# Performance work log

Measured on AMD Instinct MI355X. Metric: run time of the kernel, lower is better.

The kernel has to match this reference:

```python
import jax, jax.numpy as jnp
import numpy as np

N = 100000   # nodes
E = 1600000  # edges
IN = 32      # in_channels
H = 64       # hidden_channels
L = 16       # latent_dim
G = 64       # graphs in batch


def setup_inputs() -> dict:
    key = jax.random.key(0)
    ks = jax.random.split(key, 20)
    def w(k, shape, fan):
        return jax.random.normal(k, shape, jnp.float32) * (1.0 / np.sqrt(fan))
    inp = {}
    inp["x"] = jax.random.normal(ks[0], (N, IN), jnp.float32)
    inp["edge_index"] = jax.random.randint(ks[1], (2, E), 0, N)
    inp["batch"] = jnp.sort(jax.random.randint(ks[2], (N,), 0, G))
    # encoder GCN convs: in->h, h->h, h->h
    inp["W_enc0"] = w(ks[3], (IN, H), IN); inp["b_enc0"] = jnp.zeros((H,), jnp.float32)
    inp["W_enc1"] = w(ks[4], (H, H), H);   inp["b_enc1"] = jnp.zeros((H,), jnp.float32)
    inp["W_enc2"] = w(ks[5], (H, H), H);   inp["b_enc2"] = jnp.zeros((H,), jnp.float32)
    # latent projection and decoder projection
    inp["W_proj"] = w(ks[6], (H, L), H);   inp["b_proj"] = jnp.zeros((L,), jnp.float32)
    inp["W_dec_proj"] = w(ks[7], (L, H), L); inp["b_dec_proj"] = jnp.zeros((H,), jnp.float32)
    # decoder GCN convs: h->h, h->in
    inp["W_dec0"] = w(ks[8], (H, H), H);   inp["b_dec0"] = jnp.zeros((H,), jnp.float32)
    inp["W_dec1"] = w(ks[9], (H, IN), H);  inp["b_dec1"] = jnp.zeros((IN,), jnp.float32)
    return inp


def gcn_conv(x, W, b, src, dst, dinv):
    xw = x @ W                                   # [N, out]
    coef = (dinv[src] * dinv[dst])[:, None]      # [E, 1]
    out = jax.ops.segment_sum(xw[src] * coef, dst, num_segments=N)
    out = out + xw * (dinv * dinv)[:, None]      # self-loop contribution
    return out + b


def reference(x, edge_index, batch,
              W_enc0, b_enc0, W_enc1, b_enc1, W_enc2, b_enc2,
              W_proj, b_proj, W_dec_proj, b_dec_proj,
              W_dec0, b_dec0, W_dec1, b_dec1):
    src, dst = edge_index[0], edge_index[1]
    # degree with self-loops (computed on target nodes, PyG default)
    deg = jax.ops.segment_sum(jnp.ones((E,), jnp.float32), dst, num_segments=N) + 1.0
    dinv = jax.lax.rsqrt(deg)
    # encoder (eval mode: dropout is identity)
    h = jax.nn.relu(gcn_conv(x, W_enc0, b_enc0, src, dst, dinv))
    h = jax.nn.relu(gcn_conv(h, W_enc1, b_enc1, src, dst, dinv))
    h = jax.nn.relu(gcn_conv(h, W_enc2, b_enc2, src, dst, dinv))
    # global mean pool over graph ids
    sums = jax.ops.segment_sum(h, batch, num_segments=G)
    cnt = jax.ops.segment_sum(jnp.ones((N,), jnp.float32), batch, num_segments=G)
    g = sums / jnp.maximum(cnt, 1.0)[:, None]    # [G, H]
    z = g @ W_proj + b_proj                      # [G, L]
    # decoder: broadcast z back to nodes, project, two GCN convs
    d = jax.nn.relu(z[batch] @ W_dec_proj + b_dec_proj)
    d = jax.nn.relu(gcn_conv(d, W_dec0, b_dec0, src, dst, dinv))
    x_recon = gcn_conv(d, W_dec1, b_dec1, src, dst, dinv)
    return (x_recon, z)
```

## Files before the change

### kernel.cpp

```cpp
#include <hip/hip_runtime.h>
#include <hip/hip_bf16.h>

typedef unsigned long long u64;

static constexpr int IN_CH  = 32;
static constexpr int HID    = 64;
static constexpr int LAT    = 16;
static constexpr int NGRAPH = 64;
static constexpr int KB_CSR  = 24;
static constexpr int CPB     = 4;


__device__ inline void add4(float4& a, const float4& b) {
    a.x += b.x; a.y += b.y; a.z += b.z; a.w += b.w;
}


__global__ __launch_bounds__(256) void bhist_kernel(const int* __restrict__ ei,
                                                    int* __restrict__ bh, int E) {
    __shared__ int lh[256];
    lh[threadIdx.x] = 0;
    __syncthreads();
    int base = blockIdx.x * 2048;
    #pragma unroll
    for (int j = 0; j < 8; j++) {
        int idx = base + j * 256 + threadIdx.x;
        if (idx < E) atomicAdd(&lh[ei[E + idx] >> 9], 1);
    }
    __syncthreads();
    if (lh[threadIdx.x]) atomicAdd(&bh[threadIdx.x], lh[threadIdx.x]);
}


__global__ __launch_bounds__(256) void bin_kernel(
        const int* __restrict__ ei, const int* __restrict__ bh,
        int* __restrict__ gcur, u64* __restrict__ sout, int E) {
    __shared__ int lhist[256], lscan[256], lcur[256], gbase[256], bbaseL[256];
    __shared__ u64 sbuf[2048];
    int tid = threadIdx.x;
    lhist[tid] = 0;
    {
        int v = bh[tid];
        lscan[tid] = v;
        for (int off = 1; off < 256; off <<= 1) {
            __syncthreads();
            int x = (tid >= off) ? lscan[tid - off] : 0;
            __syncthreads();
            lscan[tid] += x;
        }
        __syncthreads();
        bbaseL[tid] = lscan[tid] - v;
    }
    __syncthreads();
    int base = blockIdx.x * 2048;
    int cnt = min(2048, E - base);
    int myb[8]; u64 myp[8];
    #pragma unroll
    for (int j = 0; j < 8; j++) {
        int idx = base + j * 256 + tid;
        myb[j] = -1;
        if (idx < E) {
            int key = ei[E + idx], val = ei[idx];
            int b = key >> 9;
            myb[j] = b;
            myp[j] = ((u64)(unsigned)key << 32) | (unsigned)val;
            atomicAdd(&lhist[b], 1);
        }
    }
    __syncthreads();
    int v = lhist[tid];
    lscan[tid] = v;
    for (int off = 1; off < 256; off <<= 1) {
        __syncthreads();
        int x = (tid >= off) ? lscan[tid - off] : 0;
        __syncthreads();
        lscan[tid] += x;
    }
    __syncthreads();
    int excl = lscan[tid] - v;
    __syncthreads();
    lscan[tid] = excl;
    lcur[tid] = excl;
    __syncthreads();
    #pragma unroll
    for (int j = 0; j < 8; j++) {
        if (myb[j] >= 0) {
            int pos = atomicAdd(&lcur[myb[j]], 1);
            sbuf[pos] = myp[j];
        }
    }
    gbase[tid] = v ? atomicAdd(&gcur[tid], v) : 0;
    __syncthreads();
    for (int i = tid; i < cnt; i += 256) {
        u64 p = sbuf[i];
        int b = (int)(p >> 41);
        sout[bbaseL[b] + gbase[b] + (i - lscan[b])] = p;
    }
}


__global__ __launch_bounds__(256) void degb_kernel(
        const u64* __restrict__ staged, const int* __restrict__ bh,
        const int* __restrict__ batch,
        int* __restrict__ rank, int* __restrict__ perm, int* __restrict__ cnt2,
        int* __restrict__ rowptr2, float* __restrict__ dinvR,
        float2* __restrict__ pgR, int* __restrict__ bbase, int N, int E) {
    __shared__ int sc[256];
    __shared__ int ldeg[512], lrank[512], degS[512], psum[512];
    __shared__ int kcur[256];
    __shared__ int s0s, s1s;
    int b = blockIdx.x, tid = threadIdx.x;
    {
        int bv = bh[tid];
        sc[tid] = bv;
        for (int off = 1; off < 256; off <<= 1) {
            __syncthreads();
            int x = (tid >= off) ? sc[tid - off] : 0;
            __syncthreads();
            sc[tid] += x;
        }
        __syncthreads();
        if (tid == b) { s0s = sc[tid] - bv; s1s = sc[tid]; }
    }
    ldeg[tid] = 0; ldeg[tid + 256] = 0;
    degS[tid] = 0; degS[tid + 256] = 0;
    kcur[tid] = 0;
    __syncthreads();
    int s0 = s0s, s1 = s1s;
    int base = b << 9;
    for (int i = s0 + tid; i < s1; i += 256)
        atomicAdd(&ldeg[(int)(__builtin_nontemporal_load(&staged[i]) >> 32) - base], 1);
    __syncthreads();
    int k = N - base; k = k < 0 ? 0 : (k > 512 ? 512 : k);
    #pragma unroll
    for (int j = 0; j < 2; j++) {
        int t = tid + j * 256;
        if (t < k) atomicAdd(&kcur[min(ldeg[t], 255)], 1);
    }
    __syncthreads();
    {
        int hv = kcur[tid];
        sc[tid] = hv;
        for (int off = 1; off < 256; off <<= 1) {
            __syncthreads();
            int x = (tid >= off) ? sc[tid - off] : 0;
            __syncthreads();
            sc[tid] += x;
        }
        __syncthreads();
        kcur[tid] = sc[tid] - hv;
    }
    __syncthreads();
    #pragma unroll
    for (int j = 0; j < 2; j++) {
        int t = tid + j * 256;
        if (t < k) lrank[t] = atomicAdd(&kcur[min(ldeg[t], 255)], 1);
    }
    __syncthreads();
    #pragma unroll
    for (int j = 0; j < 2; j++) {
        int t = tid + j * 256;
        if (t < k) degS[lrank[t]] = ldeg[t];
    }
    __syncthreads();
    {
        int v0 = degS[2 * tid], v1 = degS[2 * tid + 1];
        int T = v0 + v1;
        sc[tid] = T;
        for (int off = 1; off < 256; off <<= 1) {
            __syncthreads();
            int x = (tid >= off) ? sc[tid - off] : 0;
            __syncthreads();
            sc[tid] += x;
        }
        __syncthreads();
        int ex = sc[tid] - T;
        psum[2 * tid] = ex;
        psum[2 * tid + 1] = ex + v0;
    }
    __syncthreads();
    #pragma unroll
    for (int j = 0; j < 2; j++) {
        int t = tid + j * 256;
        if (t < k) {
            int n = base + t;
            int d = ldeg[t], lr = lrank[t];
            int r = base + lr;
            rank[n] = r;
            perm[r] = n;
            cnt2[r] = d;
            rowptr2[r] = s0 + psum[lr];
            float dv = rsqrtf((float)d + 1.0f);
            dinvR[r] = dv;
            pgR[r] = make_float2(dv, __int_as_float(batch[n]));
        }
    }
    if (tid == 0) {
        bbase[b] = s0;
        if (b == 255) bbase[256] = E;
    }
}


__global__ __launch_bounds__(256) void csr_kernel(
        const u64* __restrict__ staged, const int* __restrict__ bbase,
        const int* __restrict__ rank, const int* __restrict__ rowptr2,
        int* __restrict__ cur, int* __restrict__ col) {
    int bucket = blockIdx.x & 255;
    int k = blockIdx.x >> 8;
    int s0 = bbase[bucket], s1 = bbase[bucket + 1];
    for (int i = s0 + k * 256 + threadIdx.x; i < s1; i += 256 * KB_CSR) {
        u64 p = __builtin_nontemporal_load(&staged[i]);
        int dst = (int)(p >> 32);
        int src = (int)(p & 0xffffffffu);
        int rd = rank[dst];
        int pos = rowptr2[rd] + atomicAdd(&cur[rd], 1);
        col[pos] = rank[src];
    }
}


__global__ void slice_x_kernel(const float* __restrict__ x, const int* __restrict__ perm,
                               const float* __restrict__ dinvR,
                               float* __restrict__ xs, int N) {
    int idx = blockIdx.x * 256 + threadIdx.x;
    if (idx >= N * 2) return;
    int r = idx >> 1, h = idx & 1;
    int sl = blockIdx.y;
    int n = perm[r];
    float4 v = ((const float4*)x)[(size_t)n * 8 + sl * 2 + h];
    float dn = dinvR[r];
    v.x *= dn; v.y *= dn; v.z *= dn; v.w *= dn;
    ((float4*)(xs + (size_t)sl * N * 8))[idx] = v;
}


template <int C, bool ADD_BIAS, bool OUT_ROWMAJOR>
__global__ __launch_bounds__(256) void agg_kernel(
        const float* __restrict__ in, float* __restrict__ out,
        const int* __restrict__ rowptr2, const int* __restrict__ cnt2,
        const int* __restrict__ col, const float* __restrict__ dinvR,
        const int* __restrict__ perm, const float* __restrict__ bias,
        int nbk, int N) {
    constexpr int NSL = C / 8;
    int sl = blockIdx.x % NSL;
    int o  = blockIdx.x / NSL;
    int chunk = (o % nbk) * CPB + (o / nbk);
    int slot = threadIdx.x >> 1, h = threadIdx.x & 1;
    int r = chunk * 128 + slot;
    if (r >= N) return;
    const float4* inS = (const float4*)(in + (size_t)sl * N * 8);
    int start = rowptr2[r], m = cnt2[r];
    const int* cp = col + start;
    float4 acc = inS[(size_t)r * 2 + h];
    int i = 0;
    for (; i + 8 <= m; i += 8) {
        int s0 = cp[i], s1 = cp[i+1], s2 = cp[i+2], s3 = cp[i+3];
        int s4 = cp[i+4], s5 = cp[i+5], s6 = cp[i+6], s7 = cp[i+7];
        float4 v0 = inS[(size_t)s0*2+h], v1 = inS[(size_t)s1*2+h];
        float4 v2 = inS[(size_t)s2*2+h], v3 = inS[(size_t)s3*2+h];
        float4 v4 = inS[(size_t)s4*2+h], v5 = inS[(size_t)s5*2+h];
        float4 v6 = inS[(size_t)s6*2+h], v7 = inS[(size_t)s7*2+h];
        add4(v0, v1); add4(v2, v3); add4(v4, v5); add4(v6, v7);
        add4(v0, v2); add4(v4, v6);
        add4(acc, v0); add4(acc, v4);
    }
    if (i + 4 <= m) {
        int s0 = cp[i], s1 = cp[i+1], s2 = cp[i+2], s3 = cp[i+3];
        float4 v0 = inS[(size_t)s0*2+h], v1 = inS[(size_t)s1*2+h];
        float4 v2 = inS[(size_t)s2*2+h], v3 = inS[(size_t)s3*2+h];
        add4(v0, v1); add4(v2, v3); add4(v0, v2);
        add4(acc, v0);
        i += 4;
    }
    for (; i < m; ++i) {
        int c = cp[i];
        add4(acc, inS[(size_t)c * 2 + h]);
    }
    float dn = dinvR[r];
    acc.x *= dn; acc.y *= dn; acc.z *= dn; acc.w *= dn;
    if (ADD_BIAS) {
        float4 b4 = ((const float4*)bias)[sl * 2 + h];
        add4(acc, b4);
    }
    if (OUT_ROWMAJOR) ((float4*)out)[(size_t)perm[r] * (C / 4) + sl * 2 + h] = acc;
    else ((float4*)(out + (size_t)sl * N * 8))[(size_t)r * 2 + h] = acc;
}


__global__ __launch_bounds__(256) void gagg_kernel(
        const float* __restrict__ dg, const float2* __restrict__ pgR,
        const int* __restrict__ rowptr2, const int* __restrict__ cnt2,
        const int* __restrict__ col, float* __restrict__ out, int nbk, int N) {
    __shared__ float dgL[NGRAPH * 68];
    for (int i = threadIdx.x; i < NGRAPH * 64; i += 256)
        dgL[(i >> 6) * 68 + (i & 63)] = dg[i];
    __syncthreads();
    int slot = threadIdx.x >> 1, e = threadIdx.x & 1;
    int o = blockIdx.x;
    int chunk = (o % nbk) * CPB + (o / nbk);
    int r = chunk * 128 + slot;
    if (r >= N) return;
    const float4* dgL4 = (const float4*)dgL;
    int start = rowptr2[r], m = cnt2[r];
    const int* cp = col + start;
    float2 ps = pgR[r];
    float dn = ps.x;
    int gs = __float_as_int(ps.y);
    float4 acc[8];
    {
        const float4* rp = dgL4 + gs * 17 + e * 8;
        #pragma unroll
        for (int j = 0; j < 8; ++j) {
            float4 v = rp[j];
            acc[j] = make_float4(dn * v.x, dn * v.y, dn * v.z, dn * v.w);
        }
    }
    int i = 0;
    for (; i + 2 <= m; i += 2) {
        int c0 = cp[i], c1 = cp[i + 1];
        float2 p0 = pgR[c0], p1 = pgR[c1];
        const float4* r0 = dgL4 + __float_as_int(p0.y) * 17 + e * 8;
        const float4* r1 = dgL4 + __float_as_int(p1.y) * 17 + e * 8;
        float w0 = p0.x, w1 = p1.x;
        #pragma unroll
        for (int j = 0; j < 8; ++j) {
            float4 v0 = r0[j], v1 = r1[j];
            acc[j].x += w0 * v0.x + w1 * v1.x;
            acc[j].y += w0 * v0.y + w1 * v1.y;
            acc[j].z += w0 * v0.z + w1 * v1.z;
            acc[j].w += w0 * v0.w + w1 * v1.w;
        }
    }
    if (i < m) {
        int c0 = cp[i];
        float2 p0 = pgR[c0];
        const float4* r0 = dgL4 + __float_as_int(p0.y) * 17 + e * 8;
        float w0 = p0.x;
        #pragma unroll
        for (int j = 0; j < 8; ++j) {
            float4 v0 = r0[j];
            acc[j].x += w0 * v0.x; acc[j].y += w0 * v0.y;
            acc[j].z += w0 * v0.z; acc[j].w += w0 * v0.w;
        }
    }
    #pragma unroll
    for (int k = 0; k < 4; ++k) {
        #pragma unroll
        for (int jj = 0; jj < 2; ++jj) {
            float4 v = acc[k * 2 + jj];
            v.x *= dn; v.y *= dn; v.z *= dn; v.w *= dn;
            ((float4*)(out + (size_t)(4 * e + k) * N * 8))[(size_t)r * 2 + jj] = v;
        }
    }
}


template <int CIN, int COUT, bool RELU, bool BIAS, bool SCALE, bool OUT_ROWMAJOR>
__global__ __launch_bounds__(256) void gemm_kernel(
        const float* __restrict__ in, const float* __restrict__ W,
        const float* __restrict__ b, const float* __restrict__ dinvR,
        const int* __restrict__ perm, float* __restrict__ out, int N) {
    constexpr int NPB = 256 / COUT;
    constexpr int K4 = CIN / 4;
    __shared__ float4 xsh[NPB * K4];
    int r  = threadIdx.x / COUT;
    int co = threadIdx.x % COUT;
    float w[CIN];
    #pragma unroll
    for (int k = 0; k < CIN; ++k) w[k] = W[k * COUT + co];
    float bsv = BIAS ? b[co] : 0.f;
    int ngroups = (N + NPB - 1) / NPB;
    for (int grp = blockIdx.x; grp < ngroups; grp += gridDim.x) {
        int base = grp * NPB;
        __syncthreads();
        for (int i = threadIdx.x; i < NPB * K4; i += 256) {
            int rr = i / K4, k4 = i % K4;
            int n = base + rr;
            float4 v = make_float4(0.f, 0.f, 0.f, 0.f);
            if (n < N) v = ((const float4*)(in + (size_t)(k4 >> 1) * N * 8))[(size_t)n * 2 + (k4 & 1)];
            xsh[i] = v;
        }
        __syncthreads();
        int n = base + r;
        if (n < N) {
            float acc = bsv;
            #pragma unroll
            for (int k4 = 0; k4 < K4; ++k4) {
                float4 xv = xsh[r * K4 + k4];
                acc += xv.x * w[4 * k4] + xv.y * w[4 * k4 + 1]
                     + xv.z * w[4 * k4 + 2] + xv.w * w[4 * k4 + 3];
            }
            if (RELU) acc = fmaxf(acc, 0.f);
            if (SCALE) acc *= dinvR[n];
            if (OUT_ROWMAJOR) out[(size_t)perm[n] * COUT + co] = acc;
            else out[(size_t)(co >> 3) * N * 8 + (size_t)n * 8 + (co & 7)] = acc;
        }
    }
}


__global__ __launch_bounds__(256) void gemm2_kernel(
        const float* __restrict__ in, const float* __restrict__ W0,
        const float* __restrict__ b0, const float* __restrict__ W1,
        const float* __restrict__ dinvR, float* __restrict__ out, int N) {
    constexpr int NPB = 4;
    __shared__ float4 xsh[NPB * 16];
    __shared__ float t1sh[NPB * 65];
    __shared__ float w1sh[HID * IN_CH];
    int tid = threadIdx.x;
    int r  = tid >> 6;
    int co = tid & 63;
    float w0[HID];
    #pragma unroll
    for (int k = 0; k < HID; ++k) w0[k] = W0[k * HID + co];
    float b0v = b0[co];
    for (int i = tid; i < HID * IN_CH; i += 256) w1sh[i] = W1[i];
    int r2  = tid >> 5;
    int co2 = tid & 31;
    int ngroups = (N + NPB - 1) / NPB;
    for (int grp = blockIdx.x; grp < ngroups; grp += gridDim.x) {
        int base = grp * NPB;
        __syncthreads();
        if (tid < NPB * 16) {
            int rr = tid >> 4, k4 = tid & 15;
            int n = base + rr;
            float4 v = make_float4(0.f, 0.f, 0.f, 0.f);
            if (n < N) v = ((const float4*)(in + (size_t)(k4 >> 1) * N * 8))[(size_t)n * 2 + (k4 & 1)];
            xsh[tid] = v;
        }
        __syncthreads();
        {
            float acc = b0v;
            #pragma unroll
            for (int k4 = 0; k4 < 16; ++k4) {
                float4 xv = xsh[r * 16 + k4];
                acc += xv.x * w0[4 * k4] + xv.y * w0[4 * k4 + 1]
                     + xv.z * w0[4 * k4 + 2] + xv.w * w0[4 * k4 + 3];
            }
            t1sh[r * 65 + co] = fmaxf(acc, 0.f);
        }
        __syncthreads();
        if (r2 < NPB) {
            int n = base + r2;
            if (n < N) {
                float acc = 0.f;
                #pragma unroll
                for (int k = 0; k < HID; ++k)
                    acc += t1sh[r2 * 65 + k] * w1sh[k * IN_CH + co2];
                acc *= dinvR[n];
                out[(size_t)(co2 >> 3) * N * 8 + (size_t)n * 8 + (co2 & 7)] = acc;
            }
        }
    }
}


__global__ __launch_bounds__(256) void pool_kernel(
        const float* __restrict__ h, const int* __restrict__ batch,
        float* __restrict__ sums, int* __restrict__ cntb, int N) {
    const int CHUNK = 512;
    int chunkStart = blockIdx.x * CHUNK;
    int c = threadIdx.x & 63;
    int r = threadIdx.x >> 6;
    int curg = -1;
    float acc = 0.f;
    int cnt = 0;
    int end = chunkStart + CHUNK;
    if (end > N) end = N;
    for (int n = chunkStart + r; n < end; n += 4) {
        int g = batch[n];
        if (g != curg) {
            if (curg >= 0) {
                atomicAdd(&sums[curg * 64 + c], acc);
                if (c == 0) atomicAdd(&cntb[curg], cnt);
            }
            curg = g; acc = 0.f; cnt = 0;
        }
        acc += h[(size_t)n * 64 + c];
        cnt++;
    }
    if (curg >= 0) {
        atomicAdd(&sums[curg * 64 + c], acc);
        if (c == 0) atomicAdd(&cntb[curg], cnt);
    }
}


__global__ __launch_bounds__(1024) void latent_kernel(
        const float* __restrict__ sums, const int* __restrict__ cntb,
        const float* __restrict__ Wp, const float* __restrict__ bp,
        const float* __restrict__ Wd, const float* __restrict__ bd,
        float* __restrict__ z_out, float* __restrict__ dg) {
    __shared__ float zl[NGRAPH * LAT];
    int t = threadIdx.x;
    {
        int g = t / LAT, l = t % LAT;
        float cf = (float)cntb[g];
        float inv = 1.0f / fmaxf(cf, 1.0f);
        float acc = bp[l];
        #pragma unroll
        for (int k = 0; k < HID; k++) acc += sums[g * HID + k] * inv * Wp[k * LAT + l];
        zl[t] = acc;
        z_out[t] = acc;
    }
    __syncthreads();
    #pragma unroll
    for (int i = 0; i < 4; i++) {
        int idx = t + i * 1024;
        int g = idx >> 6, c = idx & 63;
        float acc = bd[c];
        #pragma unroll
        for (int l = 0; l < LAT; l++) acc += zl[g * LAT + l] * Wd[l * HID + c];
        dg[idx] = fmaxf(acc, 0.f);
    }
}


extern "C" void kernel_launch(void* const* d_in, const int* in_sizes, int n_in,
                              void* d_out, int out_size, void* d_ws, size_t ws_size,
                              hipStream_t stream) {
    const float* x          = (const float*)d_in[0];
    const int*   ei         = (const int*)d_in[1];
    const int*   batch      = (const int*)d_in[2];
    const float* W_enc0     = (const float*)d_in[3];
    const float* b_enc0     = (const float*)d_in[4];
    const float* W_enc1     = (const float*)d_in[5];
    const float* b_enc1     = (const float*)d_in[6];
    const float* W_enc2     = (const float*)d_in[7];
    const float* b_enc2     = (const float*)d_in[8];
    const float* W_proj     = (const float*)d_in[9];
    const float* b_proj     = (const float*)d_in[10];
    const float* W_dec_proj = (const float*)d_in[11];
    const float* b_dec_proj = (const float*)d_in[12];
    const float* W_dec0     = (const float*)d_in[13];
    const float* b_dec0     = (const float*)d_in[14];
    const float* W_dec1     = (const float*)d_in[15];
    const float* b_dec1     = (const float*)d_in[16];

    const int N = in_sizes[0] / IN_CH;
    const int E = in_sizes[1] / 2;

    char* ws = (char*)d_ws;
    size_t off = 0;
    auto alloc = [&](size_t bytes) {
        void* p = ws + off;
        off += (bytes + 255) & ~(size_t)255;
        return p;
    };
    float* A       = (float*)alloc((size_t)N * HID * 4);
    float* B       = (float*)alloc((size_t)N * HID * 4);
    float* XS      = (float*)alloc((size_t)N * IN_CH * 4);
    int*   col     = (int*)  alloc((size_t)E * 4);
    int*   cnt2    = (int*)  alloc((size_t)N * 4);
    int*   rowptr2 = (int*)  alloc((size_t)(N + 1) * 4);
    int*   perm    = (int*)  alloc((size_t)N * 4);
    int*   rank    = (int*)  alloc((size_t)N * 4);
    float* dinvR   = (float*)alloc((size_t)N * 4);
    float2* pgR    = (float2*)alloc((size_t)N * 8);
    int*   bbase   = (int*)  alloc(257 * 4);
    char* zbase = ws + off;
    int*   cursor  = (int*)  alloc((size_t)N * 4);
    int*   bh      = (int*)  alloc(256 * 4);
    int*   gcurD   = (int*)  alloc(256 * 4);
    float* sums    = (float*)alloc((size_t)NGRAPH * HID * 4);
    int*   cntb    = (int*)  alloc((size_t)NGRAPH * 4);
    size_t zbytes = (size_t)((ws + off) - zbase);
    float* dg      = (float*)alloc((size_t)NGRAPH * HID * 4);

    u64* staged1 = (u64*)XS;

    float* x_recon = (float*)d_out;
    float* z_out   = (float*)d_out + (size_t)N * IN_CH;

    hipMemsetAsync(zbase, 0, zbytes, stream);

    int ebins = (E + 2047) / 2048;
    int nbk = (N + 511) >> 9;
    int chunksI = nbk * CPB;

    bhist_kernel<<<ebins, 256, 0, stream>>>(ei, bh, E);
    bin_kernel<<<ebins, 256, 0, stream>>>(ei, bh, gcurD, staged1, E);
    degb_kernel<<<256, 256, 0, stream>>>(staged1, bh, batch, rank, perm, cnt2,
                                         rowptr2, dinvR, pgR, bbase, N, E);
    csr_kernel<<<256 * KB_CSR, 256, 0, stream>>>(staged1, bbase, rank, rowptr2, cursor, col);

    {
        dim3 g((N * 2 + 255) / 256, IN_CH / 8);
        slice_x_kernel<<<g, 256, 0, stream>>>(x, perm, dinvR, XS, N);
    }

    agg_kernel<IN_CH, false, false><<<chunksI * 4, 256, 0, stream>>>(
        XS, A, rowptr2, cnt2, col, dinvR, perm, nullptr, nbk, N);
    gemm_kernel<IN_CH, HID, true, true, true, false><<<2048, 256, 0, stream>>>(
        A, W_enc0, b_enc0, dinvR, perm, B, N);
    agg_kernel<HID, false, false><<<chunksI * 8, 256, 0, stream>>>(
        B, A, rowptr2, cnt2, col, dinvR, perm, nullptr, nbk, N);
    gemm_kernel<HID, HID, true, true, true, false><<<2048, 256, 0, stream>>>(
        A, W_enc1, b_enc1, dinvR, perm, B, N);
    agg_kernel<HID, false, false><<<chunksI * 8, 256, 0, stream>>>(
        B, A, rowptr2, cnt2, col, dinvR, perm, nullptr, nbk, N);
    gemm_kernel<HID, HID, true, true, false, true><<<2048, 256, 0, stream>>>(
        A, W_enc2, b_enc2, dinvR, perm, B, N);

    pool_kernel<<<(N + 511) / 512, 256, 0, stream>>>(B, batch, sums, cntb, N);
    latent_kernel<<<1, 1024, 0, stream>>>(sums, cntb, W_proj, b_proj, W_dec_proj, b_dec_proj, z_out, dg);

    gagg_kernel<<<chunksI, 256, 0, stream>>>(dg, pgR, rowptr2, cnt2, col, A, nbk, N);
    gemm2_kernel<<<2048, 256, 0, stream>>>(A, W_dec0, b_dec0, W_dec1, dinvR, B, N);
    agg_kernel<IN_CH, true, true><<<chunksI * 4, 256, 0, stream>>>(
        B, x_recon, rowptr2, cnt2, col, dinvR, perm, b_dec1, nbk, N);
}
```

Before: 638.7 us.

## Use shared-memory CSR cursors and widen gather unrolling in aggregation kernels

The CSR fill kernel now runs one block per 512-row bucket and keeps per-row insertion cursors in shared memory, so shared atomics replace global ones. This removes the global cursor array from the zeroed workspace, at the cost of far fewer blocks, each walking its whole bucket. The feature aggregation kernel unrolls to 16 neighbours with int4 column loads and two accumulators to raise memory-level parallelism. The decoder's graph-broadcast aggregation unrolls from 2 to 4 neighbours. The int4 loads read column indices at arbitrary offsets and rely on the hardware tolerating unaligned vector loads.

New measurement: 635.8 us. About the same (-0.5%).

```diff
diff --git a/kernel.cpp b/kernel.cpp
--- a/kernel.cpp
+++ b/kernel.cpp
@@ -7,7 +7,6 @@
 static constexpr int HID    = 64;
 static constexpr int LAT    = 16;
 static constexpr int NGRAPH = 64;
-static constexpr int KB_CSR  = 24;
 static constexpr int CPB     = 4;
 
 
@@ -205,16 +204,19 @@
 __global__ __launch_bounds__(256) void csr_kernel(
         const u64* __restrict__ staged, const int* __restrict__ bbase,
         const int* __restrict__ rank, const int* __restrict__ rowptr2,
-        int* __restrict__ cur, int* __restrict__ col) {
-    int bucket = blockIdx.x & 255;
-    int k = blockIdx.x >> 8;
-    int s0 = bbase[bucket], s1 = bbase[bucket + 1];
-    for (int i = s0 + k * 256 + threadIdx.x; i < s1; i += 256 * KB_CSR) {
+        int* __restrict__ col) {
+    __shared__ int lcur[512];
+    int b = blockIdx.x, tid = threadIdx.x;
+    lcur[tid] = 0; lcur[tid + 256] = 0;
+    __syncthreads();
+    int s0 = bbase[b], s1 = bbase[b + 1];
+    int base = b << 9;
+    for (int i = s0 + tid; i < s1; i += 256) {
         u64 p = __builtin_nontemporal_load(&staged[i]);
         int dst = (int)(p >> 32);
         int src = (int)(p & 0xffffffffu);
         int rd = rank[dst];
-        int pos = rowptr2[rd] + atomicAdd(&cur[rd], 1);
+        int pos = rowptr2[rd] + atomicAdd(&lcur[rd - base], 1);
         col[pos] = rank[src];
     }
 }
@@ -252,39 +254,61 @@
     const float4* inS = (const float4*)(in + (size_t)sl * N * 8);
     int start = rowptr2[r], m = cnt2[r];
     const int* cp = col + start;
-    float4 acc = inS[(size_t)r * 2 + h];
+    float4 acc0 = inS[(size_t)r * 2 + h];
+    float4 acc1 = make_float4(0.f, 0.f, 0.f, 0.f);
     int i = 0;
-    for (; i + 8 <= m; i += 8) {
-        int s0 = cp[i], s1 = cp[i+1], s2 = cp[i+2], s3 = cp[i+3];
-        int s4 = cp[i+4], s5 = cp[i+5], s6 = cp[i+6], s7 = cp[i+7];
-        float4 v0 = inS[(size_t)s0*2+h], v1 = inS[(size_t)s1*2+h];
-        float4 v2 = inS[(size_t)s2*2+h], v3 = inS[(size_t)s3*2+h];
-        float4 v4 = inS[(size_t)s4*2+h], v5 = inS[(size_t)s5*2+h];
-        float4 v6 = inS[(size_t)s6*2+h], v7 = inS[(size_t)s7*2+h];
+    for (; i + 16 <= m; i += 16) {
+        int4 ca = *(const int4*)(cp + i);
+        int4 cb = *(const int4*)(cp + i + 4);
+        int4 cc = *(const int4*)(cp + i + 8);
+        int4 cd = *(const int4*)(cp + i + 12);
+        float4 v0 = inS[(size_t)ca.x*2+h], v1 = inS[(size_t)ca.y*2+h];
+        float4 v2 = inS[(size_t)ca.z*2+h], v3 = inS[(size_t)ca.w*2+h];
+        float4 v4 = inS[(size_t)cb.x*2+h], v5 = inS[(size_t)cb.y*2+h];
+        float4 v6 = inS[(size_t)cb.z*2+h], v7 = inS[(size_t)cb.w*2+h];
+        float4 v8 = inS[(size_t)cc.x*2+h], v9 = inS[(size_t)cc.y*2+h];
+        float4 va = inS[(size_t)cc.z*2+h], vb = inS[(size_t)cc.w*2+h];
+        float4 vc = inS[(size_t)cd.x*2+h], vd = inS[(size_t)cd.y*2+h];
+        float4 ve = inS[(size_t)cd.z*2+h], vf = inS[(size_t)cd.w*2+h];
+        add4(v0, v1); add4(v2, v3); add4(v4, v5); add4(v6, v7);
+        add4(v8, v9); add4(va, vb); add4(vc, vd); add4(ve, vf);
+        add4(v0, v2); add4(v4, v6); add4(v8, va); add4(vc, ve);
+        add4(v0, v4); add4(v8, vc);
+        add4(acc0, v0); add4(acc1, v8);
+    }
+    if (i + 8 <= m) {
+        int4 ca = *(const int4*)(cp + i);
+        int4 cb = *(const int4*)(cp + i + 4);
+        float4 v0 = inS[(size_t)ca.x*2+h], v1 = inS[(size_t)ca.y*2+h];
+        float4 v2 = inS[(size_t)ca.z*2+h], v3 = inS[(size_t)ca.w*2+h];
+        float4 v4 = inS[(size_t)cb.x*2+h], v5 = inS[(size_t)cb.y*2+h];
+        float4 v6 = inS[(size_t)cb.z*2+h], v7 = inS[(size_t)cb.w*2+h];
         add4(v0, v1); add4(v2, v3); add4(v4, v5); add4(v6, v7);
         add4(v0, v2); add4(v4, v6);
-        add4(acc, v0); add4(acc, v4);
+        add4(acc0, v0); add4(acc1, v4);
+        i += 8;
     }
     if (i + 4 <= m) {
-        int s0 = cp[i], s1 = cp[i+1], s2 = cp[i+2], s3 = cp[i+3];
-        float4 v0 = inS[(size_t)s0*2+h], v1 = inS[(size_t)s1*2+h];
-        float4 v2 = inS[(size_t)s2*2+h], v3 = inS[(size_t)s3*2+h];
+        int4 ca = *(const int4*)(cp + i);
+        float4 v0 = inS[(size_t)ca.x*2+h], v1 = inS[(size_t)ca.y*2+h];
+        float4 v2 = inS[(size_t)ca.z*2+h], v3 = inS[(size_t)ca.w*2+h];
         add4(v0, v1); add4(v2, v3); add4(v0, v2);
-        add4(acc, v0);
+        add4(acc0, v0);
         i += 4;
     }
     for (; i < m; ++i) {
         int c = cp[i];
-        add4(acc, inS[(size_t)c * 2 + h]);
-    }
+        add4(acc1, inS[(size_t)c * 2 + h]);
+    }
+    add4(acc0, acc1);
     float dn = dinvR[r];
-    acc.x *= dn; acc.y *= dn; acc.z *= dn; acc.w *= dn;
+    acc0.x *= dn; acc0.y *= dn; acc0.z *= dn; acc0.w *= dn;
     if (ADD_BIAS) {
         float4 b4 = ((const float4*)bias)[sl * 2 + h];
-        add4(acc, b4);
-    }
-    if (OUT_ROWMAJOR) ((float4*)out)[(size_t)perm[r] * (C / 4) + sl * 2 + h] = acc;
-    else ((float4*)(out + (size_t)sl * N * 8))[(size_t)r * 2 + h] = acc;
+        add4(acc0, b4);
+    }
+    if (OUT_ROWMAJOR) ((float4*)out)[(size_t)perm[r] * (C / 4) + sl * 2 + h] = acc0;
+    else ((float4*)(out + (size_t)sl * N * 8))[(size_t)r * 2 + h] = acc0;
 }
 
 
@@ -317,22 +341,24 @@
         }
     }
     int i = 0;
-    for (; i + 2 <= m; i += 2) {
-        int c0 = cp[i], c1 = cp[i + 1];
-        float2 p0 = pgR[c0], p1 = pgR[c1];
+    for (; i + 4 <= m; i += 4) {
+        int4 ca = *(const int4*)(cp + i);
+        float2 p0 = pgR[ca.x], p1 = pgR[ca.y], p2 = pgR[ca.z], p3 = pgR[ca.w];
         const float4* r0 = dgL4 + __float_as_int(p0.y) * 17 + e * 8;
         const float4* r1 = dgL4 + __float_as_int(p1.y) * 17 + e * 8;
-        float w0 = p0.x, w1 = p1.x;
+        const float4* r2 = dgL4 + __float_as_int(p2.y) * 17 + e * 8;
+        const float4* r3 = dgL4 + __float_as_int(p3.y) * 17 + e * 8;
+        float w0 = p0.x, w1 = p1.x, w2 = p2.x, w3 = p3.x;
         #pragma unroll
         for (int j = 0; j < 8; ++j) {
-            float4 v0 = r0[j], v1 = r1[j];
-            acc[j].x += w0 * v0.x + w1 * v1.x;
-            acc[j].y += w0 * v0.y + w1 * v1.y;
-            acc[j].z += w0 * v0.z + w1 * v1.z;
-            acc[j].w += w0 * v0.w + w1 * v1.w;
-        }
-    }
-    if (i < m) {
+            float4 v0 = r0[j], v1 = r1[j], v2 = r2[j], v3 = r3[j];
+            acc[j].x += (w0 * v0.x + w1 * v1.x) + (w2 * v2.x + w3 * v3.x);
+            acc[j].y += (w0 * v0.y + w1 * v1.y) + (w2 * v2.y + w3 * v3.y);
+            acc[j].z += (w0 * v0.z + w1 * v1.z) + (w2 * v2.z + w3 * v3.z);
+            acc[j].w += (w0 * v0.w + w1 * v1.w) + (w2 * v2.w + w3 * v3.w);
+        }
+    }
+    for (; i < m; ++i) {
         int c0 = cp[i];
         float2 p0 = pgR[c0];
         const float4* r0 = dgL4 + __float_as_int(p0.y) * 17 + e * 8;
@@ -560,7 +586,6 @@
     float2* pgR    = (float2*)alloc((size_t)N * 8);
     int*   bbase   = (int*)  alloc(257 * 4);
     char* zbase = ws + off;
-    int*   cursor  = (int*)  alloc((size_t)N * 4);
     int*   bh      = (int*)  alloc(256 * 4);
     int*   gcurD   = (int*)  alloc(256 * 4);
     float* sums    = (float*)alloc((size_t)NGRAPH * HID * 4);
@@ -583,7 +608,7 @@
     bin_kernel<<<ebins, 256, 0, stream>>>(ei, bh, gcurD, staged1, E);
     degb_kernel<<<256, 256, 0, stream>>>(staged1, bh, batch, rank, perm, cnt2,
                                          rowptr2, dinvR, pgR, bbase, N, E);
-    csr_kernel<<<256 * KB_CSR, 256, 0, stream>>>(staged1, bbase, rank, rowptr2, cursor, col);
+    csr_kernel<<<256, 256, 0, stream>>>(staged1, bbase, rank, rowptr2, col);
 
     {
         dim3 g((N * 2 + 255) / 256, IN_CH / 8);
```
